# Optimization experiments

Measured on AMD Instinct MI355X. Metric: run time of the kernel, lower is better.

Reference implementation:

```python
import jax, jax.numpy as jnp
import numpy as np

EPS = 1e-6      # torch F.pairwise_distance default eps (added to the difference)
MARGIN = 0.5


def setup_inputs() -> dict:
    key = jax.random.key(0)
    k1, k2 = jax.random.split(key)
    batch = jax.random.normal(k1, (8192, 1024), dtype=jnp.float32)
    positive = jax.random.normal(k2, (1024,), dtype=jnp.float32)
    return {"batch": batch, "positive": positive}


def _loss(batch, positive):
    n, d = batch.shape
    # torch pairwise_distance(x, y) = ||x - y + eps||_2, so
    # ||a - b + eps||^2 = ||a||^2 + ||b||^2 - 2 a.b + 2*eps*(sum(a) - sum(b)) + d*eps^2
    sq = jnp.sum(batch * batch, axis=-1)                 # [n]
    dots = batch @ batch.T                               # [n, n] GEMM
    sums = jnp.sum(batch, axis=-1)                       # [n]
    d2 = (sq[:, None] + sq[None, :] - 2.0 * dots
          + 2.0 * EPS * (sums[:, None] - sums[None, :]) + d * EPS * EPS)
    # exclude self (the python loop concatenates batch[:i], batch[i+1:])
    neg_inf = jnp.asarray(-jnp.inf, d2.dtype)
    d2_masked = jnp.where(jnp.eye(n, dtype=bool), neg_inf, d2)
    max_neg = jnp.sqrt(jnp.maximum(jnp.max(d2_masked, axis=-1), 0.0))  # [n]
    # distance anchor -> positive (with torch eps convention)
    diff = batch - positive[None, :] + EPS
    pos_dist = jnp.sqrt(jnp.sum(diff * diff, axis=-1))   # [n]
    losses = jax.nn.relu(pos_dist - max_neg + MARGIN)    # [n]
    # anchors exactly equal to the positive are skipped in the original loop
    valid = ~jnp.all(batch == positive[None, :], axis=-1)
    cnt = jnp.sum(valid.astype(losses.dtype))
    return jnp.sum(jnp.where(valid, losses, 0.0)) / cnt


def reference(batch, positive):
    return _loss(batch, positive)
```

## Files before the change

### kernel.cpp

```cpp
#include <hip/hip_runtime.h>
#include <hip/hip_bf16.h>


#define NROWS 8192
#define DIM   1024
#define BT    256
#define BK    64
#define NKT   (DIM / BK)
#define NBT   (NROWS / BT)
#define NTRI  (NBT * (NBT + 1) / 2)

constexpr float EPS = 1e-6f;
constexpr float MARGIN = 0.5f;

typedef __attribute__((ext_vector_type(8))) short short8;
typedef __attribute__((ext_vector_type(4))) float f32x4;

__device__ __forceinline__ unsigned short f2bf_rne(float f) {
    unsigned u = __float_as_uint(f);
    u += 0x7fffu + ((u >> 16) & 1u);
    return (unsigned short)(u >> 16);
}

__global__ void prep_kernel(const float* __restrict__ X, const float* __restrict__ P,
                            unsigned short* __restrict__ Xb,
                            float* __restrict__ cj, float* __restrict__ basei,
                            float* __restrict__ posd, int* __restrict__ valid)
{
    const int tid  = threadIdx.x;
    const int w    = tid >> 6;
    const int lane = tid & 63;
    const int row  = blockIdx.x * 4 + w;
    const float* xr = X + (size_t)row * DIM;

    float sq = 0.f, sm = 0.f, pd = 0.f;
    bool eq = true;
    #pragma unroll
    for (int it = 0; it < 4; ++it) {
        const int idx = it * 256 + lane * 4;
        const float4 x = *(const float4*)(xr + idx);
        const float4 p = *(const float4*)(P + idx);
        sq += x.x*x.x + x.y*x.y + x.z*x.z + x.w*x.w;
        sm += x.x + x.y + x.z + x.w;
        const float d0 = x.x - p.x + EPS, d1 = x.y - p.y + EPS;
        const float d2 = x.z - p.z + EPS, d3 = x.w - p.w + EPS;
        pd += d0*d0 + d1*d1 + d2*d2 + d3*d3;
        eq = eq && (x.x == p.x) && (x.y == p.y) && (x.z == p.z) && (x.w == p.w);
        ushort4 b;
        b.x = f2bf_rne(x.x); b.y = f2bf_rne(x.y); b.z = f2bf_rne(x.z); b.w = f2bf_rne(x.w);
        *(ushort4*)(Xb + (size_t)row * DIM + idx) = b;
    }
    #pragma unroll
    for (int off = 32; off >= 1; off >>= 1) {
        sq += __shfl_xor(sq, off);
        sm += __shfl_xor(sm, off);
        pd += __shfl_xor(pd, off);
    }
    const bool alleq = __all(eq);
    if (lane == 0) {
        cj[row]    = sq - 2.f * EPS * sm;
        basei[row] = sq + 2.f * EPS * sm + (float)DIM * EPS * EPS;
        posd[row]  = sqrtf(pd);
        valid[row] = alleq ? 0 : 1;
    }
}

__global__ __launch_bounds__(512, 2) void gemm_max_kernel(
        const unsigned short* __restrict__ Xb,
        const float* __restrict__ cj,
        float* __restrict__ partmax)
{
    __shared__ alignas(16) unsigned short lds[2][4][8192];
    __shared__ float partrow[4][BT];
    __shared__ float partcol[2][BT];

    const int tid  = threadIdx.x;
    const int lane = tid & 63;
    const int wid  = tid >> 6;
    const int wm   = wid >> 2;
    const int wn   = wid & 3;
    const int l15  = lane & 15;
    const int lk   = lane >> 4;
    const int cx0  = lk ^ (l15 & 7);
    const int cx1  = (4 + lk) ^ (l15 & 7);

    const int t0 = (blockIdx.x & 7) * (NTRI / 8) + (blockIdx.x >> 3);
    int bm = (int)(32.5f - sqrtf(1056.25f - 2.f * (float)t0));
    if (bm < 0) bm = 0;
    if (bm > NBT - 1) bm = NBT - 1;
    while (bm > 0 && (65 * bm - bm * bm) / 2 > t0) --bm;
    while ((65 * (bm + 1) - (bm + 1) * (bm + 1)) / 2 <= t0) ++bm;
    const int bn = bm + (t0 - (65 * bm - bm * bm) / 2);
    const bool diag = (bm == bn);
    const int Mbase = bm * BT, Nbase = bn * BT;

    f32x4 acc[8][4];
    #pragma unroll
    for (int m = 0; m < 8; ++m)
        #pragma unroll
        for (int n = 0; n < 4; ++n)
            acc[m][n] = (f32x4){0.f, 0.f, 0.f, 0.f};

    #define STAGE(BUF, SLOT, GBASE, KT) do {                                                  \
        _Pragma("unroll")                                                                     \
        for (int inst_ = 0; inst_ < 2; ++inst_) {                                             \
            const int q_ = inst_ * 512 + tid;                                                 \
            const int r_ = q_ >> 3;                                                           \
            const int c_ = (q_ & 7) ^ (r_ & 7);                                               \
            const unsigned short* src_ = Xb + (size_t)((GBASE) + r_) * DIM + (KT) * BK + c_ * 8; \
            unsigned short* dst_ = &lds[BUF][SLOT][(inst_ * 512 + wid * 64) * 8];             \
            __builtin_amdgcn_global_load_lds((const __attribute__((address_space(1))) void*)src_, \
                                             (__attribute__((address_space(3))) void*)dst_, 16, 0, 0); \
        }                                                                                     \
    } while (0)

    STAGE(0, 0, Mbase, 0); STAGE(0, 1, Mbase + 128, 0);
    STAGE(0, 2, Nbase, 0); STAGE(0, 3, Nbase + 128, 0);
    STAGE(1, 0, Mbase, 1); STAGE(1, 1, Mbase + 128, 1);
    STAGE(1, 2, Nbase, 1); STAGE(1, 3, Nbase + 128, 1);
    asm volatile("s_waitcnt vmcnt(8)" ::: "memory");
    __builtin_amdgcn_s_barrier();
    __builtin_amdgcn_sched_barrier(0);

    const int cl0 = (wn & 1) * 64;

    for (int kt = 0; kt < NKT; ++kt) {
        const int b = kt & 1;
        const unsigned short* Ah = &lds[b][wm][0];
        const unsigned short* Bh = &lds[b][2 + (wn >> 1)][0];
        const bool st = (kt + 2 < NKT);
        const int kp = kt + 2;
        short8 af[8], bf0[4], bf1[4];

        #pragma unroll
        for (int mt = 0; mt < 4; ++mt) {
            af[mt * 2]     = *(const short8*)(Ah + (mt * 16 + l15) * 64 + cx0 * 8);
            af[mt * 2 + 1] = *(const short8*)(Ah + (mt * 16 + l15) * 64 + cx1 * 8);
        }
        #pragma unroll
        for (int nt = 0; nt < 2; ++nt) {
            bf0[nt * 2]     = *(const short8*)(Bh + (cl0 + nt * 16 + l15) * 64 + cx0 * 8);
            bf0[nt * 2 + 1] = *(const short8*)(Bh + (cl0 + nt * 16 + l15) * 64 + cx1 * 8);
        }
        __builtin_amdgcn_s_barrier();
        __builtin_amdgcn_s_setprio(1);
        #pragma unroll
        for (int mt = 0; mt < 4; ++mt)
            #pragma unroll
            for (int nt = 0; nt < 2; ++nt)
                #pragma unroll
                for (int ks = 0; ks < 2; ++ks)
                    acc[mt][nt] = __builtin_amdgcn_mfma_f32_16x16x32_bf16(af[mt*2+ks], bf0[nt*2+ks], acc[mt][nt], 0, 0, 0);
        __builtin_amdgcn_s_setprio(0);
        __builtin_amdgcn_s_barrier();

        #pragma unroll
        for (int nt = 0; nt < 2; ++nt) {
            bf1[nt * 2]     = *(const short8*)(Bh + (cl0 + 32 + nt * 16 + l15) * 64 + cx0 * 8);
            bf1[nt * 2 + 1] = *(const short8*)(Bh + (cl0 + 32 + nt * 16 + l15) * 64 + cx1 * 8);
        }
        if (st) STAGE(b, 2, Nbase, kp);
        __builtin_amdgcn_s_barrier();
        __builtin_amdgcn_s_setprio(1);
        #pragma unroll
        for (int mt = 0; mt < 4; ++mt)
            #pragma unroll
            for (int nt = 0; nt < 2; ++nt)
                #pragma unroll
                for (int ks = 0; ks < 2; ++ks)
                    acc[mt][2+nt] = __builtin_amdgcn_mfma_f32_16x16x32_bf16(af[mt*2+ks], bf1[nt*2+ks], acc[mt][2+nt], 0, 0, 0);
        __builtin_amdgcn_s_setprio(0);
        __builtin_amdgcn_s_barrier();

        #pragma unroll
        for (int mt = 0; mt < 4; ++mt) {
            af[mt * 2]     = *(const short8*)(Ah + (64 + mt * 16 + l15) * 64 + cx0 * 8);
            af[mt * 2 + 1] = *(const short8*)(Ah + (64 + mt * 16 + l15) * 64 + cx1 * 8);
        }
        if (st) STAGE(b, 3, Nbase + 128, kp);
        __builtin_amdgcn_s_barrier();
        __builtin_amdgcn_s_setprio(1);
        #pragma unroll
        for (int mt = 0; mt < 4; ++mt)
            #pragma unroll
            for (int nt = 0; nt < 2; ++nt)
                #pragma unroll
                for (int ks = 0; ks < 2; ++ks)
                    acc[4+mt][2+nt] = __builtin_amdgcn_mfma_f32_16x16x32_bf16(af[mt*2+ks], bf1[nt*2+ks], acc[4+mt][2+nt], 0, 0, 0);
        __builtin_amdgcn_s_setprio(0);
        __builtin_amdgcn_s_barrier();

        if (st) { STAGE(b, 0, Mbase, kp); STAGE(b, 1, Mbase + 128, kp); }
        __builtin_amdgcn_s_setprio(1);
        #pragma unroll
        for (int mt = 0; mt < 4; ++mt)
            #pragma unroll
            for (int nt = 0; nt < 2; ++nt)
                #pragma unroll
                for (int ks = 0; ks < 2; ++ks)
                    acc[4+mt][nt] = __builtin_amdgcn_mfma_f32_16x16x32_bf16(af[mt*2+ks], bf0[nt*2+ks], acc[4+mt][nt], 0, 0, 0);
        __builtin_amdgcn_s_setprio(0);

        if (kt < NKT - 2)       asm volatile("s_waitcnt vmcnt(8)" ::: "memory");
        else if (kt == NKT - 2) asm volatile("s_waitcnt vmcnt(0)" ::: "memory");
        __builtin_amdgcn_s_barrier();
        __builtin_amdgcn_sched_barrier(0);
    }
    #undef STAGE

    float cv[4];
    #pragma unroll
    for (int n = 0; n < 4; ++n)
        cv[n] = cj[Nbase + wn * 64 + n * 16 + l15];

    #pragma unroll
    for (int m = 0; m < 8; ++m) {
        #pragma unroll
        for (int r = 0; r < 4; ++r) {
            const int lrow = wm * 128 + m * 16 + lk * 4 + r;
            float v = -__builtin_inff();
            #pragma unroll
            for (int n = 0; n < 4; ++n) {
                float val = cv[n] - 2.f * acc[m][n][r];
                if (diag && lrow == wn * 64 + n * 16 + l15) val = -__builtin_inff();
                v = fmaxf(v, val);
            }
            #pragma unroll
            for (int off = 8; off >= 1; off >>= 1)
                v = fmaxf(v, __shfl_xor(v, off));
            if (l15 == 0) partrow[wn][lrow] = v;
        }
    }

    if (!diag) {
        float vt[4];
        #pragma unroll
        for (int n = 0; n < 4; ++n) vt[n] = -__builtin_inff();
        #pragma unroll
        for (int m = 0; m < 8; ++m) {
            #pragma unroll
            for (int r = 0; r < 4; ++r) {
                const float ci = cj[Mbase + wm * 128 + m * 16 + lk * 4 + r];
                #pragma unroll
                for (int n = 0; n < 4; ++n)
                    vt[n] = fmaxf(vt[n], ci - 2.f * acc[m][n][r]);
            }
        }
        #pragma unroll
        for (int n = 0; n < 4; ++n) {
            vt[n] = fmaxf(vt[n], __shfl_xor(vt[n], 16));
            vt[n] = fmaxf(vt[n], __shfl_xor(vt[n], 32));
            if (lk == 0) partcol[wm][wn * 64 + n * 16 + l15] = vt[n];
        }
    }
    __syncthreads();

    if (tid < BT) {
        const float v = fmaxf(fmaxf(partrow[0][tid], partrow[1][tid]),
                              fmaxf(partrow[2][tid], partrow[3][tid]));
        partmax[(size_t)bn * NROWS + Mbase + tid] = v;
    } else if (!diag) {
        const int c = tid - BT;
        partmax[(size_t)bm * NROWS + Nbase + c] = fmaxf(partcol[0][c], partcol[1][c]);
    }
}

__global__ void finalize1_kernel(const float* __restrict__ partmax,
                                 const float* __restrict__ basei,
                                 const float* __restrict__ posd,
                                 const int* __restrict__ valid,
                                 float* __restrict__ partials)
{
    const int tid = threadIdx.x;
    const int row = blockIdx.x * 256 + tid;
    float m = -__builtin_inff();
    #pragma unroll 8
    for (int p = 0; p < NBT; ++p)
        m = fmaxf(m, partmax[(size_t)p * NROWS + row]);
    const float d2 = m + basei[row];
    const float mn = sqrtf(fmaxf(d2, 0.f));
    float loss = fmaxf(posd[row] - mn + MARGIN, 0.f);
    float cnt = 1.f;
    if (!valid[row]) { loss = 0.f; cnt = 0.f; }
    #pragma unroll
    for (int off = 32; off >= 1; off >>= 1) {
        loss += __shfl_xor(loss, off);
        cnt  += __shfl_xor(cnt, off);
    }
    __shared__ float sl[4], sc[4];
    const int w = tid >> 6, lane = tid & 63;
    if (lane == 0) { sl[w] = loss; sc[w] = cnt; }
    __syncthreads();
    if (tid == 0) {
        partials[blockIdx.x * 2]     = sl[0] + sl[1] + sl[2] + sl[3];
        partials[blockIdx.x * 2 + 1] = sc[0] + sc[1] + sc[2] + sc[3];
    }
}

__global__ void finalize2_kernel(const float* __restrict__ partials, float* __restrict__ out)
{
    const int tid = threadIdx.x;
    float l = 0.f, c = 0.f;
    if (tid < 32) { l = partials[tid * 2]; c = partials[tid * 2 + 1]; }
    #pragma unroll
    for (int off = 32; off >= 1; off >>= 1) {
        l += __shfl_xor(l, off);
        c += __shfl_xor(c, off);
    }
    if (tid == 0) out[0] = l / c;
}

extern "C" void kernel_launch(void* const* d_in, const int* in_sizes, int n_in,
                              void* d_out, int out_size, void* d_ws, size_t ws_size,
                              hipStream_t stream)
{
    const float* X = (const float*)d_in[0];
    const float* P = (const float*)d_in[1];
    float* out = (float*)d_out;
    char* ws = (char*)d_ws;

    unsigned short* Xb = (unsigned short*)ws;
    size_t off = (size_t)NROWS * DIM * sizeof(unsigned short);
    float* cj    = (float*)(ws + off);  off += (size_t)NROWS * 4;
    float* basei = (float*)(ws + off);  off += (size_t)NROWS * 4;
    float* posd  = (float*)(ws + off);  off += (size_t)NROWS * 4;
    int*   valid = (int*)(ws + off);    off += (size_t)NROWS * 4;
    float* partmax = (float*)(ws + off); off += (size_t)NBT * NROWS * 4;
    float* partials = (float*)(ws + off);

    prep_kernel<<<NROWS / 4, 256, 0, stream>>>(X, P, Xb, cj, basei, posd, valid);
    gemm_max_kernel<<<NTRI, 512, 0, stream>>>(Xb, cj, partmax);
    finalize1_kernel<<<NROWS / 256, 256, 0, stream>>>(partmax, basei, posd, valid, partials);
    finalize2_kernel<<<1, 64, 0, stream>>>(partials, out);
}
```

Measured before the change: 127.8 us.

## Prefetch next-tile B fragments and drop intra-iteration barriers in the bf16 GEMM loop

Result: faster. 122.3 us (-4.3%).

```diff
diff --git a/kernel.cpp b/kernel.cpp
--- a/kernel.cpp
+++ b/kernel.cpp
@@ -124,68 +124,69 @@
 
     const int cl0 = (wn & 1) * 64;
 
+    short8 bf0[4], bf1[4], af[8];
+    {
+        const unsigned short* B0 = &lds[0][2 + (wn >> 1)][0];
+        #pragma unroll
+        for (int nt = 0; nt < 2; ++nt) {
+            bf0[nt * 2]     = *(const short8*)(B0 + ((cl0 + nt * 16 + l15) * 8 + cx0) * 8);
+            bf0[nt * 2 + 1] = *(const short8*)(B0 + ((cl0 + nt * 16 + l15) * 8 + cx1) * 8);
+        }
+    }
+
     for (int kt = 0; kt < NKT; ++kt) {
         const int b = kt & 1;
         const unsigned short* Ah = &lds[b][wm][0];
         const unsigned short* Bh = &lds[b][2 + (wn >> 1)][0];
+        const unsigned short* Bn = &lds[b ^ 1][2 + (wn >> 1)][0];
         const bool st = (kt + 2 < NKT);
         const int kp = kt + 2;
-        short8 af[8], bf0[4], bf1[4];
 
         #pragma unroll
         for (int mt = 0; mt < 4; ++mt) {
-            af[mt * 2]     = *(const short8*)(Ah + (mt * 16 + l15) * 64 + cx0 * 8);
-            af[mt * 2 + 1] = *(const short8*)(Ah + (mt * 16 + l15) * 64 + cx1 * 8);
-        }
-        #pragma unroll
-        for (int nt = 0; nt < 2; ++nt) {
-            bf0[nt * 2]     = *(const short8*)(Bh + (cl0 + nt * 16 + l15) * 64 + cx0 * 8);
-            bf0[nt * 2 + 1] = *(const short8*)(Bh + (cl0 + nt * 16 + l15) * 64 + cx1 * 8);
-        }
-        __builtin_amdgcn_s_barrier();
+            af[mt * 2]     = *(const short8*)(Ah + ((mt * 16 + l15) * 8 + cx0) * 8);
+            af[mt * 2 + 1] = *(const short8*)(Ah + ((mt * 16 + l15) * 8 + cx1) * 8);
+        }
         __builtin_amdgcn_s_setprio(1);
         #pragma unroll
-        for (int mt = 0; mt < 4; ++mt)
-            #pragma unroll
-            for (int nt = 0; nt < 2; ++nt)
-                #pragma unroll
-                for (int ks = 0; ks < 2; ++ks)
+        for (int ks = 0; ks < 2; ++ks)
+            #pragma unroll
+            for (int mt = 0; mt < 4; ++mt)
+                #pragma unroll
+                for (int nt = 0; nt < 2; ++nt)
                     acc[mt][nt] = __builtin_amdgcn_mfma_f32_16x16x32_bf16(af[mt*2+ks], bf0[nt*2+ks], acc[mt][nt], 0, 0, 0);
         __builtin_amdgcn_s_setprio(0);
         __builtin_amdgcn_s_barrier();
 
         #pragma unroll
         for (int nt = 0; nt < 2; ++nt) {
-            bf1[nt * 2]     = *(const short8*)(Bh + (cl0 + 32 + nt * 16 + l15) * 64 + cx0 * 8);
-            bf1[nt * 2 + 1] = *(const short8*)(Bh + (cl0 + 32 + nt * 16 + l15) * 64 + cx1 * 8);
-        }
-        if (st) STAGE(b, 2, Nbase, kp);
-        __builtin_amdgcn_s_barrier();
+            bf1[nt * 2]     = *(const short8*)(Bh + ((cl0 + 32 + nt * 16 + l15) * 8 + cx0) * 8);
+            bf1[nt * 2 + 1] = *(const short8*)(Bh + ((cl0 + 32 + nt * 16 + l15) * 8 + cx1) * 8);
+        }
         __builtin_amdgcn_s_setprio(1);
         #pragma unroll
-        for (int mt = 0; mt < 4; ++mt)
-            #pragma unroll
-            for (int nt = 0; nt < 2; ++nt)
-                #pragma unroll
-                for (int ks = 0; ks < 2; ++ks)
+        for (int ks = 0; ks < 2; ++ks)
+            #pragma unroll
+            for (int mt = 0; mt < 4; ++mt)
+                #pragma unroll
+                for (int nt = 0; nt < 2; ++nt)
                     acc[mt][2+nt] = __builtin_amdgcn_mfma_f32_16x16x32_bf16(af[mt*2+ks], bf1[nt*2+ks], acc[mt][2+nt], 0, 0, 0);
         __builtin_amdgcn_s_setprio(0);
         __builtin_amdgcn_s_barrier();
 
         #pragma unroll
         for (int mt = 0; mt < 4; ++mt) {
-            af[mt * 2]     = *(const short8*)(Ah + (64 + mt * 16 + l15) * 64 + cx0 * 8);
-            af[mt * 2 + 1] = *(const short8*)(Ah + (64 + mt * 16 + l15) * 64 + cx1 * 8);
-        }
-        if (st) STAGE(b, 3, Nbase + 128, kp);
-        __builtin_amdgcn_s_barrier();
+            af[mt * 2]     = *(const short8*)(Ah + ((64 + mt * 16 + l15) * 8 + cx0) * 8);
+            af[mt * 2 + 1] = *(const short8*)(Ah + ((64 + mt * 16 + l15) * 8 + cx1) * 8);
+        }
+        if (st) { STAGE(b, 2, Nbase, kp); STAGE(b, 3, Nbase + 128, kp); }
         __builtin_amdgcn_s_setprio(1);
         #pragma unroll
-        for (int mt = 0; mt < 4; ++mt)
-            #pragma unroll
-            for (int nt = 0; nt < 2; ++nt)
-                #pragma unroll
-                for (int ks = 0; ks < 2; ++ks)
+        for (int ks = 0; ks < 2; ++ks)
+            #pragma unroll
+            for (int mt = 0; mt < 4; ++mt)
+                #pragma unroll
+                for (int nt = 0; nt < 2; ++nt)
                     acc[4+mt][2+nt] = __builtin_amdgcn_mfma_f32_16x16x32_bf16(af[mt*2+ks], bf1[nt*2+ks], acc[4+mt][2+nt], 0, 0, 0);
         __builtin_amdgcn_s_setprio(0);
         __builtin_amdgcn_s_barrier();
@@ -193,16 +194,23 @@
         if (st) { STAGE(b, 0, Mbase, kp); STAGE(b, 1, Mbase + 128, kp); }
         __builtin_amdgcn_s_setprio(1);
         #pragma unroll
-        for (int mt = 0; mt < 4; ++mt)
-            #pragma unroll
-            for (int nt = 0; nt < 2; ++nt)
-                #pragma unroll
-                for (int ks = 0; ks < 2; ++ks)
+        for (int ks = 0; ks < 2; ++ks)
+            #pragma unroll
+            for (int mt = 0; mt < 4; ++mt)
+                #pragma unroll
+                for (int nt = 0; nt < 2; ++nt)
                     acc[4+mt][nt] = __builtin_amdgcn_mfma_f32_16x16x32_bf16(af[mt*2+ks], bf0[nt*2+ks], acc[4+mt][nt], 0, 0, 0);
         __builtin_amdgcn_s_setprio(0);
 
-        if (kt < NKT - 2)       asm volatile("s_waitcnt vmcnt(8)" ::: "memory");
-        else if (kt == NKT - 2) asm volatile("s_waitcnt vmcnt(0)" ::: "memory");
+        if (kt <= NKT - 3)      asm volatile("s_waitcnt vmcnt(8)" ::: "memory");
+        else                    asm volatile("s_waitcnt vmcnt(0)" ::: "memory");
+        if (kt < NKT - 1) {
+            #pragma unroll
+            for (int nt = 0; nt < 2; ++nt) {
+                bf0[nt * 2]     = *(const short8*)(Bn + ((cl0 + nt * 16 + l15) * 8 + cx0) * 8);
+                bf0[nt * 2 + 1] = *(const short8*)(Bn + ((cl0 + nt * 16 + l15) * 8 + cx1) * 8);
+            }
+        }
         __builtin_amdgcn_s_barrier();
         __builtin_amdgcn_sched_barrier(0);
     }
```

## Replace split-phase staged GEMM pipeline with simple double-buffered K loop

Applied to the files above, without the earlier changes.

New measurement: 158.9 us. +24.4%, slower.

```diff
diff --git a/kernel.cpp b/kernel.cpp
--- a/kernel.cpp
+++ b/kernel.cpp
@@ -70,7 +70,7 @@
         const float* __restrict__ cj,
         float* __restrict__ partmax)
 {
-    __shared__ alignas(16) unsigned short lds[2][4][8192];
+    __shared__ alignas(16) unsigned short lds[2][2][16384];
     __shared__ float partrow[4][BT];
     __shared__ float partcol[2][BT];
 
@@ -103,7 +103,7 @@
 
     #define STAGE(BUF, SLOT, GBASE, KT) do {                                                  \
         _Pragma("unroll")                                                                     \
-        for (int inst_ = 0; inst_ < 2; ++inst_) {                                             \
+        for (int inst_ = 0; inst_ < 4; ++inst_) {                                             \
             const int q_ = inst_ * 512 + tid;                                                 \
             const int r_ = q_ >> 3;                                                           \
             const int c_ = (q_ & 7) ^ (r_ & 7);                                               \
@@ -114,97 +114,76 @@
         }                                                                                     \
     } while (0)
 
-    STAGE(0, 0, Mbase, 0); STAGE(0, 1, Mbase + 128, 0);
-    STAGE(0, 2, Nbase, 0); STAGE(0, 3, Nbase + 128, 0);
-    STAGE(1, 0, Mbase, 1); STAGE(1, 1, Mbase + 128, 1);
-    STAGE(1, 2, Nbase, 1); STAGE(1, 3, Nbase + 128, 1);
-    asm volatile("s_waitcnt vmcnt(8)" ::: "memory");
-    __builtin_amdgcn_s_barrier();
-    __builtin_amdgcn_sched_barrier(0);
-
-    const int cl0 = (wn & 1) * 64;
-
+    STAGE(0, 0, Mbase, 0); STAGE(0, 1, Nbase, 0);
+    __syncthreads();
+
+    #pragma unroll 2
     for (int kt = 0; kt < NKT; ++kt) {
         const int b = kt & 1;
-        const unsigned short* Ah = &lds[b][wm][0];
-        const unsigned short* Bh = &lds[b][2 + (wn >> 1)][0];
-        const bool st = (kt + 2 < NKT);
-        const int kp = kt + 2;
+        if (kt + 1 < NKT) { STAGE(b ^ 1, 0, Mbase, kt + 1); STAGE(b ^ 1, 1, Nbase, kt + 1); }
+
+        const unsigned short* Ab = &lds[b][0][0];
+        const unsigned short* Bb = &lds[b][1][0];
         short8 af[8], bf0[4], bf1[4];
 
         #pragma unroll
         for (int mt = 0; mt < 4; ++mt) {
-            af[mt * 2]     = *(const short8*)(Ah + (mt * 16 + l15) * 64 + cx0 * 8);
-            af[mt * 2 + 1] = *(const short8*)(Ah + (mt * 16 + l15) * 64 + cx1 * 8);
+            const int row = wm * 128 + mt * 16 + l15;
+            af[mt * 2]     = *(const short8*)(Ab + (row * 8 + cx0) * 8);
+            af[mt * 2 + 1] = *(const short8*)(Ab + (row * 8 + cx1) * 8);
         }
         #pragma unroll
         for (int nt = 0; nt < 2; ++nt) {
-            bf0[nt * 2]     = *(const short8*)(Bh + (cl0 + nt * 16 + l15) * 64 + cx0 * 8);
-            bf0[nt * 2 + 1] = *(const short8*)(Bh + (cl0 + nt * 16 + l15) * 64 + cx1 * 8);
-        }
-        __builtin_amdgcn_s_barrier();
+            const int rowb = wn * 64 + nt * 16 + l15;
+            bf0[nt * 2]     = *(const short8*)(Bb + (rowb * 8 + cx0) * 8);
+            bf0[nt * 2 + 1] = *(const short8*)(Bb + (rowb * 8 + cx1) * 8);
+            const int rowb1 = wn * 64 + 32 + nt * 16 + l15;
+            bf1[nt * 2]     = *(const short8*)(Bb + (rowb1 * 8 + cx0) * 8);
+            bf1[nt * 2 + 1] = *(const short8*)(Bb + (rowb1 * 8 + cx1) * 8);
+        }
+
         __builtin_amdgcn_s_setprio(1);
         #pragma unroll
-        for (int mt = 0; mt < 4; ++mt)
-            #pragma unroll
-            for (int nt = 0; nt < 2; ++nt)
-                #pragma unroll
-                for (int ks = 0; ks < 2; ++ks)
+        for (int ks = 0; ks < 2; ++ks)
+            #pragma unroll
+            for (int mt = 0; mt < 4; ++mt)
+                #pragma unroll
+                for (int nt = 0; nt < 2; ++nt)
                     acc[mt][nt] = __builtin_amdgcn_mfma_f32_16x16x32_bf16(af[mt*2+ks], bf0[nt*2+ks], acc[mt][nt], 0, 0, 0);
-        __builtin_amdgcn_s_setprio(0);
-        __builtin_amdgcn_s_barrier();
-
-        #pragma unroll
-        for (int nt = 0; nt < 2; ++nt) {
-            bf1[nt * 2]     = *(const short8*)(Bh + (cl0 + 32 + nt * 16 + l15) * 64 + cx0 * 8);
-            bf1[nt * 2 + 1] = *(const short8*)(Bh + (cl0 + 32 + nt * 16 + l15) * 64 + cx1 * 8);
-        }
-        if (st) STAGE(b, 2, Nbase, kp);
-        __builtin_amdgcn_s_barrier();
-        __builtin_amdgcn_s_setprio(1);
-        #pragma unroll
-        for (int mt = 0; mt < 4; ++mt)
-            #pragma unroll
-            for (int nt = 0; nt < 2; ++nt)
-                #pragma unroll
-                for (int ks = 0; ks < 2; ++ks)
+        #pragma unroll
+        for (int ks = 0; ks < 2; ++ks)
+            #pragma unroll
+            for (int mt = 0; mt < 4; ++mt)
+                #pragma unroll
+                for (int nt = 0; nt < 2; ++nt)
                     acc[mt][2+nt] = __builtin_amdgcn_mfma_f32_16x16x32_bf16(af[mt*2+ks], bf1[nt*2+ks], acc[mt][2+nt], 0, 0, 0);
         __builtin_amdgcn_s_setprio(0);
-        __builtin_amdgcn_s_barrier();
 
         #pragma unroll
         for (int mt = 0; mt < 4; ++mt) {
-            af[mt * 2]     = *(const short8*)(Ah + (64 + mt * 16 + l15) * 64 + cx0 * 8);
-            af[mt * 2 + 1] = *(const short8*)(Ah + (64 + mt * 16 + l15) * 64 + cx1 * 8);
-        }
-        if (st) STAGE(b, 3, Nbase + 128, kp);
-        __builtin_amdgcn_s_barrier();
+            const int row = wm * 128 + 64 + mt * 16 + l15;
+            af[mt * 2]     = *(const short8*)(Ab + (row * 8 + cx0) * 8);
+            af[mt * 2 + 1] = *(const short8*)(Ab + (row * 8 + cx1) * 8);
+        }
+
         __builtin_amdgcn_s_setprio(1);
         #pragma unroll
-        for (int mt = 0; mt < 4; ++mt)
-            #pragma unroll
-            for (int nt = 0; nt < 2; ++nt)
-                #pragma unroll
-                for (int ks = 0; ks < 2; ++ks)
+        for (int ks = 0; ks < 2; ++ks)
+            #pragma unroll
+            for (int mt = 0; mt < 4; ++mt)
+                #pragma unroll
+                for (int nt = 0; nt < 2; ++nt)
+                    acc[4+mt][nt] = __builtin_amdgcn_mfma_f32_16x16x32_bf16(af[mt*2+ks], bf0[nt*2+ks], acc[4+mt][nt], 0, 0, 0);
+        #pragma unroll
+        for (int ks = 0; ks < 2; ++ks)
+            #pragma unroll
+            for (int mt = 0; mt < 4; ++mt)
+                #pragma unroll
+                for (int nt = 0; nt < 2; ++nt)
                     acc[4+mt][2+nt] = __builtin_amdgcn_mfma_f32_16x16x32_bf16(af[mt*2+ks], bf1[nt*2+ks], acc[4+mt][2+nt], 0, 0, 0);
         __builtin_amdgcn_s_setprio(0);
-        __builtin_amdgcn_s_barrier();
-
-        if (st) { STAGE(b, 0, Mbase, kp); STAGE(b, 1, Mbase + 128, kp); }
-        __builtin_amdgcn_s_setprio(1);
-        #pragma unroll
-        for (int mt = 0; mt < 4; ++mt)
-            #pragma unroll
-            for (int nt = 0; nt < 2; ++nt)
-                #pragma unroll
-                for (int ks = 0; ks < 2; ++ks)
-                    acc[4+mt][nt] = __builtin_amdgcn_mfma_f32_16x16x32_bf16(af[mt*2+ks], bf0[nt*2+ks], acc[4+mt][nt], 0, 0, 0);
-        __builtin_amdgcn_s_setprio(0);
-
-        if (kt < NKT - 2)       asm volatile("s_waitcnt vmcnt(8)" ::: "memory");
-        else if (kt == NKT - 2) asm volatile("s_waitcnt vmcnt(0)" ::: "memory");
-        __builtin_amdgcn_s_barrier();
-        __builtin_amdgcn_sched_barrier(0);
+
+        __syncthreads();
     }
     #undef STAGE
 
```
